# Kernel optimization log

Measured on AMD Instinct MI355X. Metric: run time of the kernel, lower is better.

Reference implementation:

```python
import jax, jax.numpy as jnp
import numpy as np

TOPK = 2
NUM_EXPERTS = 8


def setup_inputs() -> dict:
    key = jax.random.key(0)
    k1, k2 = jax.random.split(key)
    T, H, E = 16384, 2048, NUM_EXPERTS
    x = jax.random.normal(k1, (T, H), dtype=jnp.float32)
    W = jax.random.normal(k2, (E, H), dtype=jnp.float32) * (1.0 / np.sqrt(H))
    return {"x": x, "W": W}


def reference(x, W):
    # gating: [T, H] @ [H, E] -> [T, E]
    logits = jnp.einsum("th,eh->te", x, W)
    # top-k expert selection (largest, sorted desc, matching torch.topk)
    top_logits, top_indices = jax.lax.top_k(logits, TOPK)
    # softmax over the k selected logits, computed in fp32 (torch: dtype=float32 then type_as)
    scores = jax.nn.softmax(top_logits.astype(jnp.float32), axis=-1).astype(logits.dtype)
    # histogram of expert assignments (torch.histc -> float counts)
    tokens_per_expert = jnp.bincount(top_indices.reshape(-1), length=NUM_EXPERTS).astype(jnp.float32)
    return scores, top_indices, tokens_per_expert
```

## Files before the change

kernel.cpp:

```cpp
#include <hip/hip_runtime.h>
#include <math.h>

#define HDIM 2048
#define NEXP 8
#define TB 4
#define BLOCK 512
#define WAVES_PB 8
#define TOK_PB (WAVES_PB * TB)
#define CH 256
#define NCH (HDIM / CH)

__global__ __launch_bounds__(BLOCK, 4) void
router_main(const float* __restrict__ x,
            const float* __restrict__ W,
            float* __restrict__ out_scores,
            float* __restrict__ out_idx,
            float* __restrict__ hist,
            int T)
{
    __shared__ float wlds[NEXP][HDIM];
    __shared__ int cnt[NEXP];

    {
        const float4* __restrict__ Wv = reinterpret_cast<const float4*>(W);
        float4* wl = reinterpret_cast<float4*>(&wlds[0][0]);
#pragma unroll
        for (int j = 0; j < (NEXP * HDIM / 4) / BLOCK; ++j)
            wl[threadIdx.x + j * BLOCK] = Wv[threadIdx.x + j * BLOCK];
    }
    if (threadIdx.x < NEXP) cnt[threadIdx.x] = 0;
    __syncthreads();

    const int lane = threadIdx.x & 63;
    const int wv   = threadIdx.x >> 6;
    const int tok0 = blockIdx.x * TOK_PB + wv * TB;

    const float* xb[TB];
#pragma unroll
    for (int t = 0; t < TB; ++t) {
        int tt = tok0 + t; if (tt > T - 1) tt = T - 1;
        xb[t] = x + (size_t)tt * HDIM + lane * 4;
    }

    float acc[TB * NEXP];
#pragma unroll
    for (int i = 0; i < TB * NEXP; ++i) acc[i] = 0.f;

#pragma unroll
    for (int c = 0; c < NCH; ++c) {
        const int h = c * CH + lane * 4;
        float4 xv[TB];
#pragma unroll
        for (int t = 0; t < TB; ++t)
            xv[t] = *reinterpret_cast<const float4*>(xb[t] + c * CH);

#pragma unroll
        for (int half = 0; half < 2; ++half) {
            const int b = half * 4;
            float4 w0 = *reinterpret_cast<const float4*>(&wlds[b + 0][h]);
            float4 w1 = *reinterpret_cast<const float4*>(&wlds[b + 1][h]);
            float4 w2 = *reinterpret_cast<const float4*>(&wlds[b + 2][h]);
            float4 w3 = *reinterpret_cast<const float4*>(&wlds[b + 3][h]);
#pragma unroll
            for (int t = 0; t < TB; ++t) {
                float a0 = acc[t * NEXP + b + 0];
                float a1 = acc[t * NEXP + b + 1];
                float a2 = acc[t * NEXP + b + 2];
                float a3 = acc[t * NEXP + b + 3];
                a0 = fmaf(xv[t].x, w0.x, a0); a0 = fmaf(xv[t].y, w0.y, a0);
                a0 = fmaf(xv[t].z, w0.z, a0); a0 = fmaf(xv[t].w, w0.w, a0);
                a1 = fmaf(xv[t].x, w1.x, a1); a1 = fmaf(xv[t].y, w1.y, a1);
                a1 = fmaf(xv[t].z, w1.z, a1); a1 = fmaf(xv[t].w, w1.w, a1);
                a2 = fmaf(xv[t].x, w2.x, a2); a2 = fmaf(xv[t].y, w2.y, a2);
                a2 = fmaf(xv[t].z, w2.z, a2); a2 = fmaf(xv[t].w, w2.w, a2);
                a3 = fmaf(xv[t].x, w3.x, a3); a3 = fmaf(xv[t].y, w3.y, a3);
                a3 = fmaf(xv[t].z, w3.z, a3); a3 = fmaf(xv[t].w, w3.w, a3);
                acc[t * NEXP + b + 0] = a0;
                acc[t * NEXP + b + 1] = a1;
                acc[t * NEXP + b + 2] = a2;
                acc[t * NEXP + b + 3] = a3;
            }
        }
    }

#pragma unroll
    for (int j = 0; j < 32; ++j) acc[j] += __shfl_xor(acc[j], 32, 64);

#define FOLD(SM)                                                          \
    {                                                                     \
        const bool up = (lane & SM) != 0;                                 \
        _Pragma("unroll")                                                 \
        for (int j = 0; j < SM; ++j) {                                    \
            float keep = up ? acc[j + SM] : acc[j];                       \
            float send = up ? acc[j] : acc[j + SM];                       \
            acc[j] = keep + __shfl_xor(send, SM, 64);                     \
        }                                                                 \
    }
    FOLD(16) FOLD(8) FOLD(4) FOLD(2) FOLD(1)
#undef FOLD

    const int e_my  = lane & 7;
    const int t_loc = (lane & 31) >> 3;
    const float mylg = acc[0];

    float v1 = mylg;
    int   i1 = e_my;
#pragma unroll
    for (int m = 1; m <= 4; m <<= 1) {
        float ov = __shfl_xor(v1, m, 64);
        int   oi = __shfl_xor(i1, m, 64);
        if (ov > v1 || (ov == v1 && oi < i1)) { v1 = ov; i1 = oi; }
    }
    float v2 = (e_my == i1) ? -3.402823466e+38f : mylg;
    int   i2 = e_my;
#pragma unroll
    for (int m = 1; m <= 4; m <<= 1) {
        float ov = __shfl_xor(v2, m, 64);
        int   oi = __shfl_xor(i2, m, 64);
        if (ov > v2 || (ov == v2 && oi < i2)) { v2 = ov; i2 = oi; }
    }

    const float ed  = expf(v2 - v1);
    const float inv = 1.0f / (1.0f + ed);

    const int tok = tok0 + t_loc;
    if (lane < 32 && e_my == 0 && tok < T) {
        *reinterpret_cast<float2*>(out_scores + 2 * tok) = make_float2(inv, ed * inv);
        *reinterpret_cast<float2*>(out_idx    + 2 * tok) = make_float2((float)i1, (float)i2);
        atomicAdd(&cnt[i1], 1);
        atomicAdd(&cnt[i2], 1);
    }

    __syncthreads();
    if (threadIdx.x < NEXP)
        atomicAdd(&hist[threadIdx.x], (float)cnt[threadIdx.x]);
}

extern "C" void kernel_launch(void* const* d_in, const int* in_sizes, int n_in,
                              void* d_out, int out_size, void* d_ws, size_t ws_size,
                              hipStream_t stream)
{
    const float* x = (const float*)d_in[0];
    const float* W = (const float*)d_in[1];
    const int T = in_sizes[0] / HDIM;

    float* out        = (float*)d_out;
    float* out_scores = out;
    float* out_idx    = out + (size_t)2 * T;
    float* hist       = out + (size_t)4 * T;

    hipMemsetAsync(hist, 0, NEXP * sizeof(float), stream);

    const int nblocks = (T + TOK_PB - 1) / TOK_PB;
    router_main<<<nblocks, BLOCK, 0, stream>>>(x, W, out_scores, out_idx, hist, T);
}
```

Baseline: 42.37 us.

## Restructure x loads into token-pair phases with four chunks in flight

The main loop now processes tokens in pairs. For each pair it issues four consecutive 256-float chunk loads per token before computing, instead of loading one chunk for all four tokens at a time. The aim is more independent global loads in flight per phase while keeping the register footprint similar. The trade-off is that the LDS weight reads are repeated per token pair, doubling LDS traffic. The W staging loop is also only partially unrolled.

```diff
diff --git a/kernel.cpp b/kernel.cpp
--- a/kernel.cpp
+++ b/kernel.cpp
@@ -7,8 +7,6 @@
 #define BLOCK 512
 #define WAVES_PB 8
 #define TOK_PB (WAVES_PB * TB)
-#define CH 256
-#define NCH (HDIM / CH)
 
 __global__ __launch_bounds__(BLOCK, 4) void
 router_main(const float* __restrict__ x,
@@ -24,7 +22,7 @@
     {
         const float4* __restrict__ Wv = reinterpret_cast<const float4*>(W);
         float4* wl = reinterpret_cast<float4*>(&wlds[0][0]);
-#pragma unroll
+#pragma unroll 4
         for (int j = 0; j < (NEXP * HDIM / 4) / BLOCK; ++j)
             wl[threadIdx.x + j * BLOCK] = Wv[threadIdx.x + j * BLOCK];
     }
@@ -35,50 +33,62 @@
     const int wv   = threadIdx.x >> 6;
     const int tok0 = blockIdx.x * TOK_PB + wv * TB;
 
-    const float* xb[TB];
-#pragma unroll
-    for (int t = 0; t < TB; ++t) {
-        int tt = tok0 + t; if (tt > T - 1) tt = T - 1;
-        xb[t] = x + (size_t)tt * HDIM + lane * 4;
-    }
-
     float acc[TB * NEXP];
 #pragma unroll
     for (int i = 0; i < TB * NEXP; ++i) acc[i] = 0.f;
 
 #pragma unroll
-    for (int c = 0; c < NCH; ++c) {
-        const int h = c * CH + lane * 4;
-        float4 xv[TB];
-#pragma unroll
-        for (int t = 0; t < TB; ++t)
-            xv[t] = *reinterpret_cast<const float4*>(xb[t] + c * CH);
+    for (int p = 0; p < 2; ++p) {
+        int ta = tok0 + 2 * p;     if (ta > T - 1) ta = T - 1;
+        int tb = tok0 + 2 * p + 1; if (tb > T - 1) tb = T - 1;
+        const float* xa = x + (size_t)ta * HDIM + lane * 4;
+        const float* xb = x + (size_t)tb * HDIM + lane * 4;
 
 #pragma unroll
-        for (int half = 0; half < 2; ++half) {
-            const int b = half * 4;
-            float4 w0 = *reinterpret_cast<const float4*>(&wlds[b + 0][h]);
-            float4 w1 = *reinterpret_cast<const float4*>(&wlds[b + 1][h]);
-            float4 w2 = *reinterpret_cast<const float4*>(&wlds[b + 2][h]);
-            float4 w3 = *reinterpret_cast<const float4*>(&wlds[b + 3][h]);
+        for (int ph = 0; ph < 2; ++ph) {
+            float4 xva[4], xvb[4];
 #pragma unroll
-            for (int t = 0; t < TB; ++t) {
-                float a0 = acc[t * NEXP + b + 0];
-                float a1 = acc[t * NEXP + b + 1];
-                float a2 = acc[t * NEXP + b + 2];
-                float a3 = acc[t * NEXP + b + 3];
-                a0 = fmaf(xv[t].x, w0.x, a0); a0 = fmaf(xv[t].y, w0.y, a0);
-                a0 = fmaf(xv[t].z, w0.z, a0); a0 = fmaf(xv[t].w, w0.w, a0);
-                a1 = fmaf(xv[t].x, w1.x, a1); a1 = fmaf(xv[t].y, w1.y, a1);
-                a1 = fmaf(xv[t].z, w1.z, a1); a1 = fmaf(xv[t].w, w1.w, a1);
-                a2 = fmaf(xv[t].x, w2.x, a2); a2 = fmaf(xv[t].y, w2.y, a2);
-                a2 = fmaf(xv[t].z, w2.z, a2); a2 = fmaf(xv[t].w, w2.w, a2);
-                a3 = fmaf(xv[t].x, w3.x, a3); a3 = fmaf(xv[t].y, w3.y, a3);
-                a3 = fmaf(xv[t].z, w3.z, a3); a3 = fmaf(xv[t].w, w3.w, a3);
-                acc[t * NEXP + b + 0] = a0;
-                acc[t * NEXP + b + 1] = a1;
-                acc[t * NEXP + b + 2] = a2;
-                acc[t * NEXP + b + 3] = a3;
+            for (int c = 0; c < 4; ++c) {
+                xva[c] = *reinterpret_cast<const float4*>(xa + (4 * ph + c) * 256);
+                xvb[c] = *reinterpret_cast<const float4*>(xb + (4 * ph + c) * 256);
+            }
+#pragma unroll
+            for (int c = 0; c < 4; ++c) {
+                const int h = (4 * ph + c) * 256 + lane * 4;
+#pragma unroll
+                for (int half = 0; half < 2; ++half) {
+                    const int b = half * 4;
+                    const float4 w0 = *reinterpret_cast<const float4*>(&wlds[b + 0][h]);
+                    const float4 w1 = *reinterpret_cast<const float4*>(&wlds[b + 1][h]);
+                    const float4 w2 = *reinterpret_cast<const float4*>(&wlds[b + 2][h]);
+                    const float4 w3 = *reinterpret_cast<const float4*>(&wlds[b + 3][h]);
+
+                    const int ia = (2 * p + 0) * NEXP + b;
+                    const int ib = (2 * p + 1) * NEXP + b;
+                    float a0 = acc[ia + 0], a1 = acc[ia + 1], a2 = acc[ia + 2], a3 = acc[ia + 3];
+                    float b0 = acc[ib + 0], b1 = acc[ib + 1], b2 = acc[ib + 2], b3 = acc[ib + 3];
+
+                    a0 = fmaf(xva[c].x, w0.x, a0); a0 = fmaf(xva[c].y, w0.y, a0);
+                    a0 = fmaf(xva[c].z, w0.z, a0); a0 = fmaf(xva[c].w, w0.w, a0);
+                    a1 = fmaf(xva[c].x, w1.x, a1); a1 = fmaf(xva[c].y, w1.y, a1);
+                    a1 = fmaf(xva[c].z, w1.z, a1); a1 = fmaf(xva[c].w, w1.w, a1);
+                    a2 = fmaf(xva[c].x, w2.x, a2); a2 = fmaf(xva[c].y, w2.y, a2);
+                    a2 = fmaf(xva[c].z, w2.z, a2); a2 = fmaf(xva[c].w, w2.w, a2);
+                    a3 = fmaf(xva[c].x, w3.x, a3); a3 = fmaf(xva[c].y, w3.y, a3);
+                    a3 = fmaf(xva[c].z, w3.z, a3); a3 = fmaf(xva[c].w, w3.w, a3);
+
+                    b0 = fmaf(xvb[c].x, w0.x, b0); b0 = fmaf(xvb[c].y, w0.y, b0);
+                    b0 = fmaf(xvb[c].z, w0.z, b0); b0 = fmaf(xvb[c].w, w0.w, b0);
+                    b1 = fmaf(xvb[c].x, w1.x, b1); b1 = fmaf(xvb[c].y, w1.y, b1);
+                    b1 = fmaf(xvb[c].z, w1.z, b1); b1 = fmaf(xvb[c].w, w1.w, b1);
+                    b2 = fmaf(xvb[c].x, w2.x, b2); b2 = fmaf(xvb[c].y, w2.y, b2);
+                    b2 = fmaf(xvb[c].z, w2.z, b2); b2 = fmaf(xvb[c].w, w2.w, b2);
+                    b3 = fmaf(xvb[c].x, w3.x, b3); b3 = fmaf(xvb[c].y, w3.y, b3);
+                    b3 = fmaf(xvb[c].z, w3.z, b3); b3 = fmaf(xvb[c].w, w3.w, b3);
+
+                    acc[ia + 0] = a0; acc[ia + 1] = a1; acc[ia + 2] = a2; acc[ia + 3] = a3;
+                    acc[ib + 0] = b0; acc[ib + 1] = b1; acc[ib + 2] = b2; acc[ib + 3] = b3;
+                }
             }
         }
     }
```

Result: slower. 52.72 us (+24.4%).
